# Performance work log

Measured on AMD Instinct MI355X. Metric: run time of the kernel, lower is better.

The kernel has to match this reference:

```python
import jax, jax.numpy as jnp
import numpy as np

N, F, F1 = 8192, 256, 64
EDGE_PROB = 0.01  # adjacency density


def setup_inputs() -> dict:
    key = jax.random.key(0)
    kX, kA, kW, ka = jax.random.split(key, 4)
    X = jax.random.normal(kX, (N, F), dtype=jnp.float32)
    # binary adjacency mask (float, as in the original where A multiplies the -1e10 mask)
    A = (jax.random.uniform(kA, (N, N)) < EDGE_PROB).astype(jnp.float32)
    # glorot_uniform init for W [F1, F] and a [2, F1, 1]
    limW = float(np.sqrt(6.0 / (F1 + F)))
    W = jax.random.uniform(kW, (F1, F), minval=-limW, maxval=limW, dtype=jnp.float32)
    lima = float(np.sqrt(6.0 / (F1 + 1)))
    a = jax.random.uniform(ka, (2, F1, 1), minval=-lima, maxval=lima, dtype=jnp.float32)
    return {"X": X, "A": A, "W": W, "a": a}


def reference(X, A, W, a):
    x_features = X @ W.T                       # [N, F1]
    att_self = x_features @ a[0]               # [N, 1]
    att_neighbours = x_features @ a[1]         # [N, 1]
    att = att_self + att_neighbours.T          # [N, N] broadcast additive score
    att = jnp.where(att > 0, att, 0.2 * att)   # LeakyReLU(alpha=0.2)
    att_masked = att + (-1e10) * (1.0 - A)     # mask non-edges
    dense = jax.nn.softmax(att_masked, axis=0) # column-wise softmax (axis=0, as in source)
    return dense @ x_features                  # [N, F1]
```

## Files before the change

### kernel.cpp

```cpp
#include <hip/hip_runtime.h>
#include <math.h>

#define NN   8192
#define FF   256
#define FF1  64
#define CAP  256
#define RREP 32

__global__ __launch_bounds__(256) void k1_feat(const float* __restrict__ X,
                                               const float* __restrict__ W,
                                               const float* __restrict__ a,
                                               float* __restrict__ xf,
                                               float* __restrict__ s,
                                               float* __restrict__ t,
                                               float* __restrict__ D_rep) {
    __shared__ float Xs[32 * FF];
    const int tid  = threadIdx.x;
    const int row0 = blockIdx.x * 32;

    {
        const int gid = blockIdx.x * 256 + tid;
        ((float4*)D_rep)[gid] = make_float4(0.f, 0.f, 0.f, 0.f);
    }

    const float4* Xg  = (const float4*)(X + (size_t)row0 * FF);
    float4*       Xs4 = (float4*)Xs;
#pragma unroll
    for (int v = 0; v < 8; ++v) Xs4[tid + v * 256] = Xg[tid + v * 256];
    __syncthreads();

    const int f  = tid & 63;
    const int rg = tid >> 6;

    float acc[8] = {0.f,0.f,0.f,0.f,0.f,0.f,0.f,0.f};
    const float4* Wrow = (const float4*)(W + (size_t)f * FF);
    for (int k4 = 0; k4 < FF / 4; ++k4) {
        float4 wv = Wrow[k4];
#pragma unroll
        for (int r = 0; r < 8; ++r) {
            float4 xv = *(const float4*)&Xs[(rg * 8 + r) * FF + k4 * 4];
            acc[r] = fmaf(wv.x, xv.x, acc[r]);
            acc[r] = fmaf(wv.y, xv.y, acc[r]);
            acc[r] = fmaf(wv.z, xv.z, acc[r]);
            acc[r] = fmaf(wv.w, xv.w, acc[r]);
        }
    }

    const float a0 = a[f];
    const float a1 = a[FF1 + f];
#pragma unroll
    for (int r = 0; r < 8; ++r) {
        const int row = row0 + rg * 8 + r;
        xf[(size_t)row * FF1 + f] = acc[r];
        float vs = acc[r] * a0;
        float vt = acc[r] * a1;
#pragma unroll
        for (int off = 32; off; off >>= 1) {
            vs += __shfl_xor(vs, off);
            vt += __shfl_xor(vt, off);
        }
        if (f == 0) { s[row] = vs; t[row] = vt; }
    }
}

__global__ __launch_bounds__(256) void k2_scan(const float* __restrict__ A,
                                               unsigned short* __restrict__ idx,
                                               int* __restrict__ counts) {
    const int tid  = threadIdx.x;
    const int lane = tid & 63;
    const int wv   = tid >> 6;
    __shared__ unsigned short lbuf[256 * 8];
    __shared__ int wtot[4];

    for (int r = 0; r < 4; ++r) {
        const int i = blockIdx.x * 4 + r;
        int c = 0;
        const float4* Arow = (const float4*)(A + (size_t)i * NN);
#pragma unroll
        for (int k = 0; k < 8; ++k) {
            const int v = tid + k * 256;
            float4 av = Arow[v];
            if (av.x != 0.f) { lbuf[tid * 8 + (c & 7)] = (unsigned short)(4 * v + 0); ++c; }
            if (av.y != 0.f) { lbuf[tid * 8 + (c & 7)] = (unsigned short)(4 * v + 1); ++c; }
            if (av.z != 0.f) { lbuf[tid * 8 + (c & 7)] = (unsigned short)(4 * v + 2); ++c; }
            if (av.w != 0.f) { lbuf[tid * 8 + (c & 7)] = (unsigned short)(4 * v + 3); ++c; }
        }
        if (c > 8) c = 8;

        int sc = c;
#pragma unroll
        for (int off = 1; off < 64; off <<= 1) {
            int n = __shfl_up(sc, off);
            if (lane >= off) sc += n;
        }
        if (lane == 63) wtot[wv] = sc;
        __syncthreads();

        int base = sc - c;
#pragma unroll
        for (int w = 0; w < 4; ++w) if (w < wv) base += wtot[w];

        for (int q = 0; q < c; ++q) {
            const int pos = base + q;
            if (pos < CAP) idx[(size_t)i * CAP + pos] = lbuf[tid * 8 + q];
        }
        if (tid == 255) {
            const int total = base + c;
            counts[i] = (total < CAP) ? total : CAP;
        }
        __syncthreads();
    }
}

__global__ __launch_bounds__(256) void k2b_edge(const float* __restrict__ s,
                                                const float* __restrict__ t,
                                                const unsigned short* __restrict__ idx,
                                                const int* __restrict__ counts,
                                                float* __restrict__ ev,
                                                float* __restrict__ D_rep) {
    const int wv   = threadIdx.x >> 6;
    const int lane = threadIdx.x & 63;
    const int i    = blockIdx.x * 4 + wv;
    float* __restrict__ Dr = D_rep + (size_t)(blockIdx.x & (RREP - 1)) * NN;

    const int   cnt = counts[i];
    const float si  = s[i];
    for (int p = lane; p < cnt; p += 64) {
        const int j = idx[(size_t)i * CAP + p];
        const float x  = si + t[j];
        const float lr = x > 0.f ? x : 0.2f * x;
        const float e  = __expf(lr);
        ev[(size_t)i * CAP + p] = e;
        atomicAdd(&Dr[j], e);
    }
}

__global__ __launch_bounds__(256) void k2c_reduce(const float* __restrict__ D_rep,
                                                  float* __restrict__ D) {
    const int j = blockIdx.x * 256 + threadIdx.x;
    float sum = 0.f;
#pragma unroll
    for (int r = 0; r < RREP; ++r) sum += D_rep[(size_t)r * NN + j];
    D[j] = sum;
}

__global__ __launch_bounds__(256) void k3_apply(const float* __restrict__ xf,
                                                const float* __restrict__ D,
                                                const unsigned short* __restrict__ idx,
                                                const float* __restrict__ ev,
                                                const int* __restrict__ counts,
                                                float* __restrict__ out) {
    const int wave = threadIdx.x >> 6;
    const int lane = threadIdx.x & 63;
    const int i    = blockIdx.x * 4 + wave;

    const int cnt = counts[i];
    float acc0 = 0.f, acc1 = 0.f, acc2 = 0.f, acc3 = 0.f;

    for (int base = 0; base < cnt; base += 64) {
        const int p = base + lane;
        const bool act = (p < cnt);
        int   j = act ? (int)idx[(size_t)i * CAP + p] : 0;
        float w = act ? ev[(size_t)i * CAP + p] / D[j] : 0.f;

#pragma unroll
        for (int e = 0; e < 64; e += 4) {
            {
                const int   je = __builtin_amdgcn_readlane(j, e + 0);
                const float we = __int_as_float(__builtin_amdgcn_readlane(__float_as_int(w), e + 0));
                acc0 = fmaf(we, xf[(size_t)je * FF1 + lane], acc0);
            }
            {
                const int   je = __builtin_amdgcn_readlane(j, e + 1);
                const float we = __int_as_float(__builtin_amdgcn_readlane(__float_as_int(w), e + 1));
                acc1 = fmaf(we, xf[(size_t)je * FF1 + lane], acc1);
            }
            {
                const int   je = __builtin_amdgcn_readlane(j, e + 2);
                const float we = __int_as_float(__builtin_amdgcn_readlane(__float_as_int(w), e + 2));
                acc2 = fmaf(we, xf[(size_t)je * FF1 + lane], acc2);
            }
            {
                const int   je = __builtin_amdgcn_readlane(j, e + 3);
                const float we = __int_as_float(__builtin_amdgcn_readlane(__float_as_int(w), e + 3));
                acc3 = fmaf(we, xf[(size_t)je * FF1 + lane], acc3);
            }
        }
    }
    out[(size_t)i * FF1 + lane] = (acc0 + acc1) + (acc2 + acc3);
}

extern "C" void kernel_launch(void* const* d_in, const int* in_sizes, int n_in,
                              void* d_out, int out_size, void* d_ws, size_t ws_size,
                              hipStream_t stream) {
    const float* X = (const float*)d_in[0];
    const float* A = (const float*)d_in[1];
    const float* W = (const float*)d_in[2];
    const float* a = (const float*)d_in[3];
    float* out = (float*)d_out;

    char* ws = (char*)d_ws;
    float* xf = (float*)ws;                                  ws += (size_t)NN * FF1 * 4;
    float* s  = (float*)ws;                                  ws += (size_t)NN * 4;
    float* t  = (float*)ws;                                  ws += (size_t)NN * 4;
    float* D  = (float*)ws;                                  ws += (size_t)NN * 4;
    int*   counts = (int*)ws;                                ws += (size_t)NN * 4;
    unsigned short* idx = (unsigned short*)ws;               ws += (size_t)NN * CAP * 2;
    float* ev = (float*)ws;                                  ws += (size_t)NN * CAP * 4;
    float* D_rep = (float*)ws;

    k1_feat<<<NN / 32, 256, 0, stream>>>(X, W, a, xf, s, t, D_rep);
    k2_scan<<<NN / 4, 256, 0, stream>>>(A, idx, counts);
    k2b_edge<<<NN / 4, 256, 0, stream>>>(s, t, idx, counts, ev, D_rep);
    k2c_reduce<<<NN / 256, 256, 0, stream>>>(D_rep, D);
    k3_apply<<<NN / 4, 256, 0, stream>>>(xf, D, idx, ev, counts, out);
}
```

Before: 111.4 us.

## Pre-scale features by column softmax denominator and use unsafe float atomics

```diff
diff --git a/kernel.cpp b/kernel.cpp
--- a/kernel.cpp
+++ b/kernel.cpp
@@ -131,21 +131,26 @@
         const float lr = x > 0.f ? x : 0.2f * x;
         const float e  = __expf(lr);
         ev[(size_t)i * CAP + p] = e;
-        atomicAdd(&Dr[j], e);
-    }
-}
-
-__global__ __launch_bounds__(256) void k2c_reduce(const float* __restrict__ D_rep,
-                                                  float* __restrict__ D) {
-    const int j = blockIdx.x * 256 + threadIdx.x;
-    float sum = 0.f;
-#pragma unroll
-    for (int r = 0; r < RREP; ++r) sum += D_rep[(size_t)r * NN + j];
-    D[j] = sum;
-}
-
-__global__ __launch_bounds__(256) void k3_apply(const float* __restrict__ xf,
-                                                const float* __restrict__ D,
+        unsafeAtomicAdd(&Dr[j], e);
+    }
+}
+
+__global__ __launch_bounds__(256) void k2c_yf(const float* __restrict__ D_rep,
+                                              const float* __restrict__ xf,
+                                              float* __restrict__ yf) {
+    const int wv   = threadIdx.x >> 6;
+    const int lane = threadIdx.x & 63;
+    const int j    = blockIdx.x * 4 + wv;
+
+    float d = (lane < RREP) ? D_rep[(size_t)lane * NN + j] : 0.f;
+#pragma unroll
+    for (int off = 16; off; off >>= 1) d += __shfl_xor(d, off);
+    d = __shfl(d, 0);
+    const float rD = 1.0f / d;
+    yf[(size_t)j * FF1 + lane] = xf[(size_t)j * FF1 + lane] * rD;
+}
+
+__global__ __launch_bounds__(256) void k3_apply(const float* __restrict__ yf,
                                                 const unsigned short* __restrict__ idx,
                                                 const float* __restrict__ ev,
                                                 const int* __restrict__ counts,
@@ -161,29 +166,29 @@
         const int p = base + lane;
         const bool act = (p < cnt);
         int   j = act ? (int)idx[(size_t)i * CAP + p] : 0;
-        float w = act ? ev[(size_t)i * CAP + p] / D[j] : 0.f;
+        float w = act ? ev[(size_t)i * CAP + p] : 0.f;
 
 #pragma unroll
         for (int e = 0; e < 64; e += 4) {
             {
                 const int   je = __builtin_amdgcn_readlane(j, e + 0);
                 const float we = __int_as_float(__builtin_amdgcn_readlane(__float_as_int(w), e + 0));
-                acc0 = fmaf(we, xf[(size_t)je * FF1 + lane], acc0);
+                acc0 = fmaf(we, yf[(size_t)je * FF1 + lane], acc0);
             }
             {
                 const int   je = __builtin_amdgcn_readlane(j, e + 1);
                 const float we = __int_as_float(__builtin_amdgcn_readlane(__float_as_int(w), e + 1));
-                acc1 = fmaf(we, xf[(size_t)je * FF1 + lane], acc1);
+                acc1 = fmaf(we, yf[(size_t)je * FF1 + lane], acc1);
             }
             {
                 const int   je = __builtin_amdgcn_readlane(j, e + 2);
                 const float we = __int_as_float(__builtin_amdgcn_readlane(__float_as_int(w), e + 2));
-                acc2 = fmaf(we, xf[(size_t)je * FF1 + lane], acc2);
+                acc2 = fmaf(we, yf[(size_t)je * FF1 + lane], acc2);
             }
             {
                 const int   je = __builtin_amdgcn_readlane(j, e + 3);
                 const float we = __int_as_float(__builtin_amdgcn_readlane(__float_as_int(w), e + 3));
-                acc3 = fmaf(we, xf[(size_t)je * FF1 + lane], acc3);
+                acc3 = fmaf(we, yf[(size_t)je * FF1 + lane], acc3);
             }
         }
     }
@@ -201,9 +206,9 @@
 
     char* ws = (char*)d_ws;
     float* xf = (float*)ws;                                  ws += (size_t)NN * FF1 * 4;
+    float* yf = (float*)ws;                                  ws += (size_t)NN * FF1 * 4;
     float* s  = (float*)ws;                                  ws += (size_t)NN * 4;
     float* t  = (float*)ws;                                  ws += (size_t)NN * 4;
-    float* D  = (float*)ws;                                  ws += (size_t)NN * 4;
     int*   counts = (int*)ws;                                ws += (size_t)NN * 4;
     unsigned short* idx = (unsigned short*)ws;               ws += (size_t)NN * CAP * 2;
     float* ev = (float*)ws;                                  ws += (size_t)NN * CAP * 4;
@@ -212,6 +217,6 @@
     k1_feat<<<NN / 32, 256, 0, stream>>>(X, W, a, xf, s, t, D_rep);
     k2_scan<<<NN / 4, 256, 0, stream>>>(A, idx, counts);
     k2b_edge<<<NN / 4, 256, 0, stream>>>(s, t, idx, counts, ev, D_rep);
-    k2c_reduce<<<NN / 256, 256, 0, stream>>>(D_rep, D);
-    k3_apply<<<NN / 4, 256, 0, stream>>>(xf, D, idx, ev, counts, out);
-}
+    k2c_yf<<<NN / 4, 256, 0, stream>>>(D_rep, xf, yf);
+    k3_apply<<<NN / 4, 256, 0, stream>>>(yf, idx, ev, counts, out);
+}
```

New measurement: 109.7 us. No clear change (-1.5%).
